# Kernel tuning notes

Measured on AMD Instinct MI355X. Metric: run time of the kernel, lower is better.

## Reference

```python
import jax, jax.numpy as jnp
import numpy as np

# Bernstein-basis theta coefficients for d=2 (calculate_theta2(2)),
# inv_coeff order: [x^0, x^1, x^2]
THETAS = ((3.0, -3.0, 0.75), (0.0, 3.0, -1.5), (0.0, 0.0, 0.75))
HIGH_ORDER = 2

N_NODES = 50000
N_EDGES = 800000
IN_DIM, HID_DIM, OUT_DIM = 128, 64, 2


def setup_inputs() -> dict:
    key = jax.random.key(0)
    ks = jax.random.split(key, 16)
    f32 = jnp.float32
    def w(k, shape, fan_in):
        return jax.random.normal(k, shape, dtype=f32) * (1.0 / np.sqrt(fan_in))
    return {
        "in_feat": jax.random.normal(ks[0], (N_NODES, IN_DIM), dtype=f32),
        "src": jax.random.randint(ks[1], (N_EDGES,), 0, N_NODES, dtype=jnp.int32),
        "dst": jax.random.randint(ks[2], (N_EDGES,), 0, N_NODES, dtype=jnp.int32),
        "W1": w(ks[3], (IN_DIM, HID_DIM), IN_DIM), "b1": jnp.zeros((HID_DIM,), f32),
        "W2": w(ks[4], (HID_DIM, HID_DIM), HID_DIM), "b2": jnp.zeros((HID_DIM,), f32),
        "W3": w(ks[5], (HID_DIM * 5, HID_DIM), HID_DIM * 5), "b3": jnp.zeros((HID_DIM,), f32),
        "W4": w(ks[6], (HID_DIM, OUT_DIM), HID_DIM), "b4": jnp.zeros((OUT_DIM,), f32),
        "Wg1": w(ks[7], (IN_DIM, HID_DIM), IN_DIM), "bg1": jnp.zeros((HID_DIM,), f32),
        "Wg2": w(ks[8], (HID_DIM, IN_DIM), HID_DIM), "bg2": jnp.zeros((IN_DIM,), f32),
    }


def _spmm(x, src, dst, n):
    # y[v] = sum_{(u,v) in E} x[u]   (DGL update_all(copy_u, sum))
    return jax.ops.segment_sum(x[src], dst, num_segments=n)


def reference(in_feat, src, dst, W1, b1, W2, b2, W3, b3, W4, b4, Wg1, bg1, Wg2, bg2):
    n = in_feat.shape[0]
    ones_e = jnp.ones(src.shape[0], dtype=in_feat.dtype)
    deg_in = jnp.clip(jax.ops.segment_sum(ones_e, dst, num_segments=n), 1.0)
    deg_out = jnp.clip(jax.ops.segment_sum(ones_e, src, num_segments=n), 1.0)
    din = (deg_in ** -0.5)[:, None]   # [N,1]
    dout = (deg_out ** -0.5)[:, None]

    def lap(f):
        # f - D^{-1/2} A D^{-1/2} f  (in-degree norm, as in unnLaplacian)
        return f - _spmm(f * din, src, dst, n) * din

    # MLP front-end
    h = jax.nn.relu(in_feat @ W1 + b1)
    h = jax.nn.relu(h @ W2 + b2)

    branches = []
    # BandConv branches (lin=False): theta-weighted Laplacian polynomial
    for theta in THETAS:
        f = h
        acc = theta[0] * h
        for k in range(1, len(theta)):
            f = lap(f)
            acc = acc + theta[k] * f
        branches.append(acc)
    # HighConv branches: repeated Laplacian, num_layer = 1..HIGH_ORDER
    f = h
    for j in range(HIGH_ORDER):
        f = lap(f)
        branches.append(f)

    h_final = jnp.concatenate(branches, axis=-1)  # [N, 5*hid]
    out = jax.nn.relu(h_final @ W3 + b3) @ W4 + b4  # [N, out_dim]

    # GCN branch on self-loop-free graph (same edges here): symmetric norm GraphConv
    def gconv(x, W, b):
        return _spmm(x * dout, src, dst, n) * din @ W + b
    emb = gconv(jax.nn.relu(gconv(in_feat, Wg1, bg1)), Wg2, bg2)  # [N, in_dim]

    return out, emb
```

## Files before the change

kernel.cpp:

```cpp
#include <hip/hip_runtime.h>
#include <hip/hip_bf16.h>
#include <math.h>

#define NN 50000
#define NE 800000
#define C64 64
#define CE 12500
#define RW2 6250
#define NW 25000
#define HISTB 256
#define INITB 160
#define RB 98
#define GB 782
#define ZSB 782
#define FSG 3125
#define FSB 6250

typedef _Float16 half8 __attribute__((ext_vector_type(8)));
typedef _Float16 half4v __attribute__((ext_vector_type(4)));
typedef float f32x4 __attribute__((ext_vector_type(4)));
typedef unsigned short ushort4v __attribute__((ext_vector_type(4)));

static inline int cdiv(int a, int b) { return (a + b - 1) / b; }


__device__ inline size_t pack_pos(int k, int n, int K, int M) {
    int tile = n >> 4;
    int kstep = k >> 5;
    int quad = (k >> 3) & 3;
    int j = k & 7;
    int lane = (quad << 4) | (n & 15);
    return ((size_t)(tile * (K >> 5) + kstep) * 64 + lane) * 8 + j;
}

__device__ void pack_std_dev(int bx, const float* __restrict__ W, _Float16* __restrict__ Wpk,
                             int K, int M) {
    int idx = bx * 256 + threadIdx.x;
    if (idx >= K * M) return;
    int k = idx / M, n = idx % M;
    Wpk[pack_pos(k, n, K, M)] = (_Float16)W[idx];
}

__device__ void pack_wc_dev(int bx, const float* __restrict__ W3, _Float16* __restrict__ wcpk) {
    int idx = bx * 256 + threadIdx.x;
    if (idx >= 3 * 4096) return;
    int b = idx >> 12;
    int rem = idx & 4095;
    int k = rem >> 6, n = rem & 63;
    float w0 = W3[(0 * 64 + k) * 64 + n];
    float w1 = W3[(1 * 64 + k) * 64 + n];
    float w2 = W3[(2 * 64 + k) * 64 + n];
    float w3 = W3[(3 * 64 + k) * 64 + n];
    float w4 = W3[(4 * 64 + k) * 64 + n];
    float v;
    if (b == 0)      v = 3.f * w0;
    else if (b == 1) v = -3.f * w0 + 3.f * w1 + w3;
    else             v = 0.75f * w0 - 1.5f * w1 + 0.75f * w2 + w4;
    wcpk[pack_pos(b * 64 + k, n, 192, 64)] = (_Float16)v;
}

__device__ void init_dev(int bx,
                         const float* __restrict__ W1, _Float16* __restrict__ W1pk,
                         const float* __restrict__ W2, _Float16* __restrict__ W2pk,
                         const float* __restrict__ Wg1, _Float16* __restrict__ Wg1pk,
                         const float* __restrict__ Wg2, _Float16* __restrict__ Wg2pk,
                         const float* __restrict__ W3, _Float16* __restrict__ wcpk) {
    if (bx < 32) { pack_std_dev(bx, W1, W1pk, 128, 64); return; }
    bx -= 32;
    if (bx < 16) { pack_std_dev(bx, W2, W2pk, 64, 64); return; }
    bx -= 16;
    if (bx < 32) { pack_std_dev(bx, Wg1, Wg1pk, 128, 64); return; }
    bx -= 32;
    if (bx < 32) { pack_std_dev(bx, Wg2, Wg2pk, 64, 128); return; }
    bx -= 32;
    pack_wc_dev(bx, W3, wcpk);
}


__device__ void hist_dev(int bx, const int* __restrict__ idx, unsigned* __restrict__ H,
                         unsigned* __restrict__ cnt) {
    int c = bx & 63, r = bx >> 6;
    int tid = threadIdx.x;
    for (int j = tid; j < RW2; j += 256) cnt[j] = 0;
    __syncthreads();
    int lo = r * 12500;
    const int* p = idx + (size_t)c * CE;
    for (int i = tid; i < CE; i += 256) {
        int v = p[i] - lo;
        if ((unsigned)v < 12500u)
            atomicAdd(&cnt[v >> 1], 1u << ((v & 1) * 16));
    }
    __syncthreads();
    unsigned* outp = H + (size_t)c * NW + r * RW2;
    for (int j = tid; j < RW2; j += 256) outp[j] = cnt[j];
}

__device__ void reduce_dev(int bx, const unsigned* __restrict__ H, int* __restrict__ dgo,
                           float* __restrict__ o_rsq, float* __restrict__ o_inv,
                           float* __restrict__ o_sq) {
    int w = bx * 256 + threadIdx.x;
    if (w >= NW) return;
    unsigned slo = 0, shi = 0;
#pragma unroll 8
    for (int c = 0; c < C64; c++) {
        unsigned h = H[(size_t)c * NW + w];
        slo += h & 0xffffu; shi += h >> 16;
    }
    if (dgo) {
        dgo[2 * w]     = slo > 64u ? 64 : (int)slo;
        dgo[2 * w + 1] = shi > 64u ? 64 : (int)shi;
    }
    float f0 = (float)(slo < 1u ? 1u : slo);
    float f1 = (float)(shi < 1u ? 1u : shi);
    o_rsq[2 * w] = rsqrtf(f0); o_rsq[2 * w + 1] = rsqrtf(f1);
    if (o_inv) { o_inv[2 * w] = 1.f / f0; o_inv[2 * w + 1] = 1.f / f1; }
    if (o_sq)  { o_sq[2 * w] = sqrtf(f0); o_sq[2 * w + 1] = sqrtf(f1); }
}

__device__ void prefix_dev(int bx, const unsigned* __restrict__ HD, unsigned* __restrict__ baseD) {
    int w = bx * 256 + threadIdx.x;
    if (w >= NW) return;
    unsigned slo = 0, shi = 0;
    for (int c = 0; c < C64; c++) {
        unsigned b0 = slo > 64u ? 64u : slo;
        unsigned b1 = shi > 64u ? 64u : shi;
        baseD[(size_t)c * NW + w] = b0 | (b1 << 16);
        unsigned h = HD[(size_t)c * NW + w];
        slo += h & 0xffffu; shi += h >> 16;
    }
}

__device__ void scatter_dev(int bx, const int* __restrict__ src, const int* __restrict__ dst,
                            const unsigned* __restrict__ baseD,
                            unsigned short* __restrict__ colsPad,
                            unsigned* __restrict__ cnt) {
    int c = bx & 63, r = bx >> 6;
    int tid = threadIdx.x;
    const unsigned* bslice = baseD + (size_t)c * NW + r * RW2;
    for (int j = tid; j < RW2; j += 256) cnt[j] = bslice[j];
    __syncthreads();
    int lo = r * 12500;
    const int* pd = dst + (size_t)c * CE;
    const int* ps = src + (size_t)c * CE;
    for (int i = tid; i < CE; i += 256) {
        int v = pd[i];
        int lv = v - lo;
        if ((unsigned)lv < 12500u) {
            int sh = (lv & 1) * 16;
            unsigned old = atomicAdd(&cnt[lv >> 1], 1u << sh);
            unsigned pos = (old >> sh) & 0xffffu;
            if (pos < 64u) colsPad[(size_t)v * 64 + pos] = (unsigned short)ps[i];
        }
    }
}

__device__ void zscale_dev(int bx, half8* __restrict__ zh8, const float* __restrict__ dout, int N) {
    int idx = bx * 256 + threadIdx.x;
    if (idx >= N * 4) return;
    int row = idx >> 2;
    float m = dout[row];
    half8 a = zh8[idx * 2], b = zh8[idx * 2 + 1];
#pragma unroll
    for (int j = 0; j < 8; j++) {
        a[j] = (_Float16)((float)a[j] * m);
        b[j] = (_Float16)((float)b[j] * m);
    }
    zh8[idx * 2] = a; zh8[idx * 2 + 1] = b;
}


struct HSegs { const _Float16* p[3]; int ld[3]; };

template <int M, int K, bool OUTW, bool RSCA>
__device__ void mg_dev(int bx, HSegs A, const half8* __restrict__ Wpk,
                       const float* __restrict__ bias, int relu,
                       float* __restrict__ C,
                       _Float16* __restrict__ Ch0, const float* __restrict__ ms0,
                       const float* __restrict__ rsc,
                       const float* __restrict__ W4, const float* __restrict__ b4,
                       float* __restrict__ outp, int N) {
    constexpr int NT = M / 16;
    constexpr int NKS = K / 32;
    int tid = threadIdx.x;
    int wave = tid >> 6, lane = tid & 63;
    int quad = lane >> 4, m = lane & 15;
    int row0 = bx * 64 + wave * 16;
    int rowA = row0 + m; if (rowA >= N) rowA = N - 1;
    _Float16 hs = (_Float16)1.f;
    if (RSCA) hs = (_Float16)rsc[rowA];
    f32x4 acc[NT];
#pragma unroll
    for (int t = 0; t < NT; t++) acc[t] = (f32x4){0.f, 0.f, 0.f, 0.f};
#pragma unroll
    for (int ks = 0; ks < NKS; ks++) {
        const _Float16* ap = A.p[ks >> 1] + (size_t)rowA * A.ld[ks >> 1] + (ks & 1) * 32 + quad * 8;
        half8 af = *(const half8*)ap;
        if (RSCA) {
#pragma unroll
            for (int j = 0; j < 8; j++) af[j] *= hs;
        }
#pragma unroll
        for (int t = 0; t < NT; t++) {
            half8 bf = Wpk[(t * NKS + ks) * 64 + lane];
            acc[t] = __builtin_amdgcn_mfma_f32_16x16x32_f16(af, bf, acc[t], 0, 0, 0);
        }
    }
    float outv[NT][4];
#pragma unroll
    for (int t = 0; t < NT; t++) {
        float bv = bias ? bias[t * 16 + m] : 0.f;
#pragma unroll
        for (int r = 0; r < 4; r++) {
            float v = acc[t][r] + bv;
            if (relu) v = fmaxf(v, 0.f);
            outv[t][r] = v;
        }
    }
    if (OUTW) {
        float w40[NT], w41[NT];
#pragma unroll
        for (int t = 0; t < NT; t++) {
            w40[t] = W4[(t * 16 + m) * 2];
            w41[t] = W4[(t * 16 + m) * 2 + 1];
        }
#pragma unroll
        for (int r = 0; r < 4; r++) {
            float p0 = 0.f, p1 = 0.f;
#pragma unroll
            for (int t = 0; t < NT; t++) {
                p0 += outv[t][r] * w40[t];
                p1 += outv[t][r] * w41[t];
            }
#pragma unroll
            for (int off = 1; off < 16; off <<= 1) {
                p0 += __shfl_xor(p0, off);
                p1 += __shfl_xor(p1, off);
            }
            int row = row0 + quad * 4 + r;
            if (m == 0 && row < N) {
                outp[(size_t)row * 2 + 0] = p0 + b4[0];
                outp[(size_t)row * 2 + 1] = p1 + b4[1];
            }
        }
    }
    if (C || Ch0) {
#pragma unroll
        for (int r = 0; r < 4; r++) {
            int row = row0 + quad * 4 + r;
            if (row >= N) continue;
            float m0 = (Ch0 && ms0) ? ms0[row] : 1.f;
#pragma unroll
            for (int t = 0; t < NT; t++) {
                size_t off = (size_t)row * M + t * 16 + m;
                if (C)   C[off] = outv[t][r];
                if (Ch0) Ch0[off] = (_Float16)(outv[t][r] * m0);
            }
        }
    }
}

__device__ void a15_dev(int bx, const float* __restrict__ in_feat,
                        const half8* __restrict__ W1pk, const half8* __restrict__ Wg1pk,
                        const float* __restrict__ b1,
                        _Float16* __restrict__ h1h, _Float16* __restrict__ zh, int N) {
    int tid = threadIdx.x;
    int wave = tid >> 6, lane = tid & 63;
    int quad = lane >> 4, m = lane & 15;
    int row0 = bx * 64 + wave * 16;
    int rowA = row0 + m; if (rowA >= N) rowA = N - 1;
    f32x4 acc0[4], acc1[4];
#pragma unroll
    for (int t = 0; t < 4; t++) {
        acc0[t] = (f32x4){0.f, 0.f, 0.f, 0.f};
        acc1[t] = (f32x4){0.f, 0.f, 0.f, 0.f};
    }
#pragma unroll
    for (int ks = 0; ks < 4; ks++) {
        const float* ap = in_feat + (size_t)rowA * 128 + ks * 32 + quad * 8;
        float4 u = *(const float4*)ap;
        float4 v = *(const float4*)(ap + 4);
        half8 af;
        af[0] = (_Float16)u.x; af[1] = (_Float16)u.y; af[2] = (_Float16)u.z; af[3] = (_Float16)u.w;
        af[4] = (_Float16)v.x; af[5] = (_Float16)v.y; af[6] = (_Float16)v.z; af[7] = (_Float16)v.w;
#pragma unroll
        for (int t = 0; t < 4; t++) {
            acc0[t] = __builtin_amdgcn_mfma_f32_16x16x32_f16(af, W1pk[(t * 4 + ks) * 64 + lane], acc0[t], 0, 0, 0);
            acc1[t] = __builtin_amdgcn_mfma_f32_16x16x32_f16(af, Wg1pk[(t * 4 + ks) * 64 + lane], acc1[t], 0, 0, 0);
        }
    }
#pragma unroll
    for (int r = 0; r < 4; r++) {
        int row = row0 + quad * 4 + r;
        if (row >= N) continue;
#pragma unroll
        for (int t = 0; t < 4; t++) {
            float v0 = fmaxf(acc0[t][r] + b1[t * 16 + m], 0.f);
            h1h[(size_t)row * 64 + t * 16 + m] = (_Float16)v0;
            zh[(size_t)row * 64 + t * 16 + m] = (_Float16)acc1[t][r];
        }
    }
}


__launch_bounds__(256)
__global__ void k_L1(const float* __restrict__ W1, _Float16* __restrict__ W1pk,
                     const float* __restrict__ W2, _Float16* __restrict__ W2pk,
                     const float* __restrict__ Wg1, _Float16* __restrict__ Wg1pk,
                     const float* __restrict__ Wg2, _Float16* __restrict__ Wg2pk,
                     const float* __restrict__ W3, _Float16* __restrict__ wcpk,
                     const int* __restrict__ src, const int* __restrict__ dst,
                     unsigned* __restrict__ HD, unsigned* __restrict__ HS) {
    __shared__ unsigned cnt[RW2];
    int bx = blockIdx.x;
    if (bx < INITB) { init_dev(bx, W1, W1pk, W2, W2pk, Wg1, Wg1pk, Wg2, Wg2pk, W3, wcpk); return; }
    bx -= INITB;
    if (bx < HISTB) { hist_dev(bx, dst, HD, cnt); return; }
    bx -= HISTB;
    hist_dev(bx, src, HS, cnt);
}

__launch_bounds__(256)
__global__ void k_L2(const unsigned* __restrict__ HD, const unsigned* __restrict__ HS,
                     int* __restrict__ degin, float* __restrict__ din,
                     float* __restrict__ din2, float* __restrict__ dsq,
                     float* __restrict__ dout, unsigned* __restrict__ baseD,
                     const float* __restrict__ in_feat,
                     const half8* __restrict__ W1pk, const half8* __restrict__ Wg1pk,
                     const float* __restrict__ b1,
                     _Float16* __restrict__ h1h, _Float16* __restrict__ zh, int N) {
    int bx = blockIdx.x;
    if (bx < RB) { reduce_dev(bx, HD, degin, din, din2, dsq); return; }
    bx -= RB;
    if (bx < RB) { reduce_dev(bx, HS, nullptr, dout, nullptr, nullptr); return; }
    bx -= RB;
    if (bx < RB) { prefix_dev(bx, HD, baseD); return; }
    bx -= RB;
    a15_dev(bx, in_feat, W1pk, Wg1pk, b1, h1h, zh, N);
}

__launch_bounds__(256)
__global__ void k_L3(const int* __restrict__ src, const int* __restrict__ dst,
                     const unsigned* __restrict__ baseD, unsigned short* __restrict__ colsPad,
                     const _Float16* __restrict__ h1h, const half8* __restrict__ W2pk,
                     const float* __restrict__ b2, _Float16* __restrict__ u0h,
                     const float* __restrict__ din,
                     half8* __restrict__ zh8, const float* __restrict__ dout, int N) {
    __shared__ unsigned cnt[RW2];
    int bx = blockIdx.x;
    if (bx < HISTB) { scatter_dev(bx, src, dst, baseD, colsPad, cnt); return; }
    bx -= HISTB;
    if (bx < GB) {
        HSegs A;
        A.p[0] = h1h; A.ld[0] = 64;
        A.p[1] = nullptr; A.ld[1] = 0;
        A.p[2] = nullptr; A.ld[2] = 0;
        mg_dev<64, 64, false, false>(bx, A, W2pk, b2, 1, nullptr, u0h, din,
                                     nullptr, nullptr, nullptr, nullptr, N);
        return;
    }
    bx -= GB;
    zscale_dev(bx, zh8, dout, N);
}


struct SpmmP {
    const half4v* xh; const half4v* fsub_h; const float* rowscale; const float* bias;
    half4v* yh0; const float* ms0; int relu;
};

__launch_bounds__(256)
__global__ void k_FS(SpmmP P0, SpmmP P1, const unsigned short* __restrict__ colsPad,
                     const int* __restrict__ deg, int N) {
    int bx = blockIdx.x;
    bool first = bx < FSG;
    SpmmP P = first ? P0 : P1;
    int g = first ? bx : bx - FSG;
    int tid = threadIdx.x;
    int wave = tid >> 6, lane = tid & 63;
    int quad = lane >> 4, c = lane & 15;
    int row = g * 16 + wave * 4 + quad;
    if (row >= N) return;
    int dg = deg[row];
    const unsigned short* cp = colsPad + (size_t)row * 64;
    float ax = 0.f, ay = 0.f, az = 0.f, aw = 0.f;
    int e = 0;
    for (; e + 7 < dg; e += 8) {
        ushort4v sa = *(const ushort4v*)(cp + e);
        ushort4v sb = *(const ushort4v*)(cp + e + 4);
        half4v v0 = P.xh[(size_t)sa.x * 16 + c];
        half4v v1 = P.xh[(size_t)sa.y * 16 + c];
        half4v v2 = P.xh[(size_t)sa.z * 16 + c];
        half4v v3 = P.xh[(size_t)sa.w * 16 + c];
        half4v v4 = P.xh[(size_t)sb.x * 16 + c];
        half4v v5 = P.xh[(size_t)sb.y * 16 + c];
        half4v v6 = P.xh[(size_t)sb.z * 16 + c];
        half4v v7 = P.xh[(size_t)sb.w * 16 + c];
        ax += (float)v0.x + (float)v1.x + (float)v2.x + (float)v3.x
            + (float)v4.x + (float)v5.x + (float)v6.x + (float)v7.x;
        ay += (float)v0.y + (float)v1.y + (float)v2.y + (float)v3.y
            + (float)v4.y + (float)v5.y + (float)v6.y + (float)v7.y;
        az += (float)v0.z + (float)v1.z + (float)v2.z + (float)v3.z
            + (float)v4.z + (float)v5.z + (float)v6.z + (float)v7.z;
        aw += (float)v0.w + (float)v1.w + (float)v2.w + (float)v3.w
            + (float)v4.w + (float)v5.w + (float)v6.w + (float)v7.w;
    }
    for (; e + 3 < dg; e += 4) {
        ushort4v ss = *(const ushort4v*)(cp + e);
        half4v v0 = P.xh[(size_t)ss.x * 16 + c];
        half4v v1 = P.xh[(size_t)ss.y * 16 + c];
        half4v v2 = P.xh[(size_t)ss.z * 16 + c];
        half4v v3 = P.xh[(size_t)ss.w * 16 + c];
        ax += (float)v0.x + (float)v1.x + (float)v2.x + (float)v3.x;
        ay += (float)v0.y + (float)v1.y + (float)v2.y + (float)v3.y;
        az += (float)v0.z + (float)v1.z + (float)v2.z + (float)v3.z;
        aw += (float)v0.w + (float)v1.w + (float)v2.w + (float)v3.w;
    }
    for (; e < dg; e++) {
        int s = cp[e];
        half4v v = P.xh[(size_t)s * 16 + c];
        ax += (float)v.x; ay += (float)v.y; az += (float)v.z; aw += (float)v.w;
    }
    size_t oidx = (size_t)row * 16 + c;
    if (P.fsub_h) {
        float d = P.rowscale[row];
        half4v f = P.fsub_h[oidx];
        ax = (float)f.x - ax * d; ay = (float)f.y - ay * d;
        az = (float)f.z - az * d; aw = (float)f.w - aw * d;
    } else {
        if (P.rowscale) { float d = P.rowscale[row]; ax *= d; ay *= d; az *= d; aw *= d; }
        if (P.bias) {
            float4 bb = ((const float4*)P.bias)[c];
            ax += bb.x; ay += bb.y; az += bb.z; aw += bb.w;
        }
        if (P.relu) {
            ax = fmaxf(ax, 0.f); ay = fmaxf(ay, 0.f);
            az = fmaxf(az, 0.f); aw = fmaxf(aw, 0.f);
        }
    }
    float mm = P.ms0 ? P.ms0[row] : 1.f;
    half4v h;
    h.x = (_Float16)(ax * mm); h.y = (_Float16)(ay * mm);
    h.z = (_Float16)(az * mm); h.w = (_Float16)(aw * mm);
    P.yh0[oidx] = h;
}

__launch_bounds__(256)
__global__ void k_F3(const _Float16* __restrict__ u0h, const _Float16* __restrict__ u1h,
                     const _Float16* __restrict__ u2h, const half8* __restrict__ wcpk,
                     const float* __restrict__ b3, const float* __restrict__ dsq,
                     const float* __restrict__ W4, const float* __restrict__ b4,
                     float* __restrict__ outp,
                     const _Float16* __restrict__ sgh, const half8* __restrict__ Wg2pk,
                     const float* __restrict__ bg2, float* __restrict__ emb, int N) {
    int bx = blockIdx.x;
    if (bx < GB) {
        HSegs A;
        A.p[0] = u0h; A.ld[0] = 64;
        A.p[1] = u1h; A.ld[1] = 64;
        A.p[2] = u2h; A.ld[2] = 64;
        mg_dev<64, 192, true, true>(bx, A, wcpk, b3, 1, nullptr, nullptr, nullptr,
                                    dsq, W4, b4, outp, N);
        return;
    }
    bx -= GB;
    HSegs A;
    A.p[0] = sgh; A.ld[0] = 64;
    A.p[1] = nullptr; A.ld[1] = 0;
    A.p[2] = nullptr; A.ld[2] = 0;
    mg_dev<128, 64, false, false>(bx, A, Wg2pk, bg2, 0, emb, nullptr, nullptr,
                                  nullptr, nullptr, nullptr, nullptr, N);
}

extern "C" void kernel_launch(void* const* d_in, const int* in_sizes, int n_in,
                              void* d_out, int out_size, void* d_ws, size_t ws_size,
                              hipStream_t stream) {
    const int N = NN;
    const float* in_feat = (const float*)d_in[0];
    const int* src = (const int*)d_in[1];
    const int* dst = (const int*)d_in[2];
    const float* W1 = (const float*)d_in[3];
    const float* b1 = (const float*)d_in[4];
    const float* W2 = (const float*)d_in[5];
    const float* b2 = (const float*)d_in[6];
    const float* W3 = (const float*)d_in[7];
    const float* b3 = (const float*)d_in[8];
    const float* W4 = (const float*)d_in[9];
    const float* b4 = (const float*)d_in[10];
    const float* Wg1 = (const float*)d_in[11];
    const float* bg1 = (const float*)d_in[12];
    const float* Wg2 = (const float*)d_in[13];
    const float* bg2 = (const float*)d_in[14];

    float* out = (float*)d_out;
    float* emb = out + (size_t)N * 2;

    float* fw = (float*)d_ws;
    float* din  = fw;
    float* din2 = din + N;
    float* dsq  = din2 + N;
    float* dout = dsq + N;
    int* degin  = (int*)(dout + N);
    unsigned short* colsPad = (unsigned short*)(degin + N);
    unsigned* HD   = (unsigned*)(colsPad + (size_t)64 * N);
    unsigned* HS   = HD + (size_t)C64 * NW;
    unsigned* baseD = HS + (size_t)C64 * NW;
    _Float16* hp = (_Float16*)(baseD + (size_t)C64 * NW);
    _Float16* h1h   = hp;
    _Float16* u0h   = h1h + (size_t)64 * N;
    _Float16* u1h   = u0h + (size_t)64 * N;
    _Float16* u2h   = u1h + (size_t)64 * N;
    _Float16* zh    = u2h + (size_t)64 * N;
    _Float16* g1h   = zh + (size_t)64 * N;
    _Float16* sgh   = g1h + (size_t)64 * N;
    _Float16* W1pk  = sgh + (size_t)64 * N;
    _Float16* W2pk  = W1pk + 8192;
    _Float16* Wg1pk = W2pk + 4096;
    _Float16* Wg2pk = Wg1pk + 8192;
    _Float16* wcpk  = Wg2pk + 8192;

    k_L1<<<INITB + 2 * HISTB, 256, 0, stream>>>(W1, W1pk, W2, W2pk, Wg1, Wg1pk,
        Wg2, Wg2pk, W3, wcpk, src, dst, HD, HS);

    k_L2<<<3 * RB + GB, 256, 0, stream>>>(HD, HS, degin, din, din2, dsq, dout, baseD,
        in_feat, (const half8*)W1pk, (const half8*)Wg1pk, b1, h1h, zh, N);

    k_L3<<<HISTB + GB + ZSB, 256, 0, stream>>>(src, dst, baseD, colsPad,
        h1h, (const half8*)W2pk, b2, u0h, din, (half8*)zh, dout, N);

    SpmmP p0, p1;
    p0 = {(const half4v*)u0h, (const half4v*)u0h, din2, nullptr, (half4v*)u1h, nullptr, 0};
    p1 = {(const half4v*)zh, nullptr, din, bg1, (half4v*)g1h, dout, 1};
    k_FS<<<FSB, 256, 0, stream>>>(p0, p1, colsPad, degin, N);

    p0 = {(const half4v*)u1h, (const half4v*)u1h, din2, nullptr, (half4v*)u2h, nullptr, 0};
    p1 = {(const half4v*)g1h, nullptr, nullptr, nullptr, (half4v*)sgh, din, 0};
    k_FS<<<FSB, 256, 0, stream>>>(p0, p1, colsPad, degin, N);

    k_F3<<<2 * GB, 256, 0, stream>>>(u0h, u1h, u2h, (const half8*)wcpk, b3, dsq,
        W4, b4, out, sgh, (const half8*)Wg2pk, bg2, emb, N);
}
```

Before: 259.4 us.

## Build padded CSR with global atomics instead of chunked LDS histograms

Replaces the multi-pass adjacency build (per-chunk LDS histograms for in- and out-degree, a 64-chunk reduction, a prefix pass and a chunked LDS scatter) with one pass over the edges. Each thread does global atomicAdd on per-node in- and out-degree counters and writes the source index into the padded column slot returned by the dst atomic. The large intermediate histogram and base arrays are removed. The kernel that used to run the scatter now runs only the GEMM and zscale work, and a memset is added to zero the counters. In exchange, neighbour order within each row becomes nondeterministic, and the build depends on global-atomic throughput and on contention for high-degree nodes.

```diff
diff --git a/kernel.cpp b/kernel.cpp
--- a/kernel.cpp
+++ b/kernel.cpp
@@ -4,13 +4,9 @@
 
 #define NN 50000
 #define NE 800000
-#define C64 64
-#define CE 12500
-#define RW2 6250
-#define NW 25000
-#define HISTB 256
+#define BLD 3125
+#define NORMB 196
 #define INITB 160
-#define RB 98
 #define GB 782
 #define ZSB 782
 #define FSG 3125
@@ -77,81 +73,32 @@
 }
 
 
-__device__ void hist_dev(int bx, const int* __restrict__ idx, unsigned* __restrict__ H,
-                         unsigned* __restrict__ cnt) {
-    int c = bx & 63, r = bx >> 6;
-    int tid = threadIdx.x;
-    for (int j = tid; j < RW2; j += 256) cnt[j] = 0;
-    __syncthreads();
-    int lo = r * 12500;
-    const int* p = idx + (size_t)c * CE;
-    for (int i = tid; i < CE; i += 256) {
-        int v = p[i] - lo;
-        if ((unsigned)v < 12500u)
-            atomicAdd(&cnt[v >> 1], 1u << ((v & 1) * 16));
-    }
-    __syncthreads();
-    unsigned* outp = H + (size_t)c * NW + r * RW2;
-    for (int j = tid; j < RW2; j += 256) outp[j] = cnt[j];
-}
-
-__device__ void reduce_dev(int bx, const unsigned* __restrict__ H, int* __restrict__ dgo,
-                           float* __restrict__ o_rsq, float* __restrict__ o_inv,
-                           float* __restrict__ o_sq) {
-    int w = bx * 256 + threadIdx.x;
-    if (w >= NW) return;
-    unsigned slo = 0, shi = 0;
-#pragma unroll 8
-    for (int c = 0; c < C64; c++) {
-        unsigned h = H[(size_t)c * NW + w];
-        slo += h & 0xffffu; shi += h >> 16;
-    }
-    if (dgo) {
-        dgo[2 * w]     = slo > 64u ? 64 : (int)slo;
-        dgo[2 * w + 1] = shi > 64u ? 64 : (int)shi;
-    }
-    float f0 = (float)(slo < 1u ? 1u : slo);
-    float f1 = (float)(shi < 1u ? 1u : shi);
-    o_rsq[2 * w] = rsqrtf(f0); o_rsq[2 * w + 1] = rsqrtf(f1);
-    if (o_inv) { o_inv[2 * w] = 1.f / f0; o_inv[2 * w + 1] = 1.f / f1; }
-    if (o_sq)  { o_sq[2 * w] = sqrtf(f0); o_sq[2 * w + 1] = sqrtf(f1); }
-}
-
-__device__ void prefix_dev(int bx, const unsigned* __restrict__ HD, unsigned* __restrict__ baseD) {
-    int w = bx * 256 + threadIdx.x;
-    if (w >= NW) return;
-    unsigned slo = 0, shi = 0;
-    for (int c = 0; c < C64; c++) {
-        unsigned b0 = slo > 64u ? 64u : slo;
-        unsigned b1 = shi > 64u ? 64u : shi;
-        baseD[(size_t)c * NW + w] = b0 | (b1 << 16);
-        unsigned h = HD[(size_t)c * NW + w];
-        slo += h & 0xffffu; shi += h >> 16;
-    }
-}
-
-__device__ void scatter_dev(int bx, const int* __restrict__ src, const int* __restrict__ dst,
-                            const unsigned* __restrict__ baseD,
-                            unsigned short* __restrict__ colsPad,
-                            unsigned* __restrict__ cnt) {
-    int c = bx & 63, r = bx >> 6;
-    int tid = threadIdx.x;
-    const unsigned* bslice = baseD + (size_t)c * NW + r * RW2;
-    for (int j = tid; j < RW2; j += 256) cnt[j] = bslice[j];
-    __syncthreads();
-    int lo = r * 12500;
-    const int* pd = dst + (size_t)c * CE;
-    const int* ps = src + (size_t)c * CE;
-    for (int i = tid; i < CE; i += 256) {
-        int v = pd[i];
-        int lv = v - lo;
-        if ((unsigned)lv < 12500u) {
-            int sh = (lv & 1) * 16;
-            unsigned old = atomicAdd(&cnt[lv >> 1], 1u << sh);
-            unsigned pos = (old >> sh) & 0xffffu;
-            if (pos < 64u) colsPad[(size_t)v * 64 + pos] = (unsigned short)ps[i];
-        }
-    }
+__device__ void build_dev(int bx, const int* __restrict__ src, const int* __restrict__ dst,
+                          int* __restrict__ cntD, int* __restrict__ cntS,
+                          unsigned short* __restrict__ colsPad) {
+    int i = bx * 256 + threadIdx.x;
+    int s = src[i];
+    int v = dst[i];
+    atomicAdd(&cntS[s], 1);
+    int pos = atomicAdd(&cntD[v], 1);
+    if (pos < 64) colsPad[(size_t)v * 64 + pos] = (unsigned short)s;
+}
+
+__device__ void norm_dev(int bx, const int* __restrict__ cntD, const int* __restrict__ cntS,
+                         int* __restrict__ degin, float* __restrict__ din,
+                         float* __restrict__ din2, float* __restrict__ dsq,
+                         float* __restrict__ dout) {
+    int i = bx * 256 + threadIdx.x;
+    if (i >= NN) return;
+    int d = cntD[i];
+    degin[i] = d > 64 ? 64 : d;
+    float f = (float)(d < 1 ? 1 : d);
+    din[i] = rsqrtf(f);
+    din2[i] = 1.f / f;
+    dsq[i] = sqrtf(f);
+    int o = cntS[i];
+    float g = (float)(o < 1 ? 1 : o);
+    dout[i] = rsqrtf(g);
 }
 
 __device__ void zscale_dev(int bx, half8* __restrict__ zh8, const float* __restrict__ dout, int N) {
@@ -303,52 +250,41 @@
 
 
 __launch_bounds__(256)
-__global__ void k_L1(const float* __restrict__ W1, _Float16* __restrict__ W1pk,
-                     const float* __restrict__ W2, _Float16* __restrict__ W2pk,
-                     const float* __restrict__ Wg1, _Float16* __restrict__ Wg1pk,
-                     const float* __restrict__ Wg2, _Float16* __restrict__ Wg2pk,
-                     const float* __restrict__ W3, _Float16* __restrict__ wcpk,
-                     const int* __restrict__ src, const int* __restrict__ dst,
-                     unsigned* __restrict__ HD, unsigned* __restrict__ HS) {
-    __shared__ unsigned cnt[RW2];
+__global__ void k_B(const float* __restrict__ W1, _Float16* __restrict__ W1pk,
+                    const float* __restrict__ W2, _Float16* __restrict__ W2pk,
+                    const float* __restrict__ Wg1, _Float16* __restrict__ Wg1pk,
+                    const float* __restrict__ Wg2, _Float16* __restrict__ Wg2pk,
+                    const float* __restrict__ W3, _Float16* __restrict__ wcpk,
+                    const int* __restrict__ src, const int* __restrict__ dst,
+                    int* __restrict__ cntD, int* __restrict__ cntS,
+                    unsigned short* __restrict__ colsPad) {
     int bx = blockIdx.x;
     if (bx < INITB) { init_dev(bx, W1, W1pk, W2, W2pk, Wg1, Wg1pk, Wg2, Wg2pk, W3, wcpk); return; }
     bx -= INITB;
-    if (bx < HISTB) { hist_dev(bx, dst, HD, cnt); return; }
-    bx -= HISTB;
-    hist_dev(bx, src, HS, cnt);
+    build_dev(bx, src, dst, cntD, cntS, colsPad);
 }
 
 __launch_bounds__(256)
-__global__ void k_L2(const unsigned* __restrict__ HD, const unsigned* __restrict__ HS,
+__global__ void k_L2(const int* __restrict__ cntD, const int* __restrict__ cntS,
                      int* __restrict__ degin, float* __restrict__ din,
                      float* __restrict__ din2, float* __restrict__ dsq,
-                     float* __restrict__ dout, unsigned* __restrict__ baseD,
+                     float* __restrict__ dout,
                      const float* __restrict__ in_feat,
                      const half8* __restrict__ W1pk, const half8* __restrict__ Wg1pk,
                      const float* __restrict__ b1,
                      _Float16* __restrict__ h1h, _Float16* __restrict__ zh, int N) {
     int bx = blockIdx.x;
-    if (bx < RB) { reduce_dev(bx, HD, degin, din, din2, dsq); return; }
-    bx -= RB;
-    if (bx < RB) { reduce_dev(bx, HS, nullptr, dout, nullptr, nullptr); return; }
-    bx -= RB;
-    if (bx < RB) { prefix_dev(bx, HD, baseD); return; }
-    bx -= RB;
+    if (bx < NORMB) { norm_dev(bx, cntD, cntS, degin, din, din2, dsq, dout); return; }
+    bx -= NORMB;
     a15_dev(bx, in_feat, W1pk, Wg1pk, b1, h1h, zh, N);
 }
 
 __launch_bounds__(256)
-__global__ void k_L3(const int* __restrict__ src, const int* __restrict__ dst,
-                     const unsigned* __restrict__ baseD, unsigned short* __restrict__ colsPad,
-                     const _Float16* __restrict__ h1h, const half8* __restrict__ W2pk,
+__global__ void k_L3(const _Float16* __restrict__ h1h, const half8* __restrict__ W2pk,
                      const float* __restrict__ b2, _Float16* __restrict__ u0h,
                      const float* __restrict__ din,
                      half8* __restrict__ zh8, const float* __restrict__ dout, int N) {
-    __shared__ unsigned cnt[RW2];
     int bx = blockIdx.x;
-    if (bx < HISTB) { scatter_dev(bx, src, dst, baseD, colsPad, cnt); return; }
-    bx -= HISTB;
     if (bx < GB) {
         HSegs A;
         A.p[0] = h1h; A.ld[0] = 64;
@@ -500,11 +436,10 @@
     float* dsq  = din2 + N;
     float* dout = dsq + N;
     int* degin  = (int*)(dout + N);
-    unsigned short* colsPad = (unsigned short*)(degin + N);
-    unsigned* HD   = (unsigned*)(colsPad + (size_t)64 * N);
-    unsigned* HS   = HD + (size_t)C64 * NW;
-    unsigned* baseD = HS + (size_t)C64 * NW;
-    _Float16* hp = (_Float16*)(baseD + (size_t)C64 * NW);
+    int* cntD   = degin + N;
+    int* cntS   = cntD + N;
+    unsigned short* colsPad = (unsigned short*)(cntS + N);
+    _Float16* hp = (_Float16*)(colsPad + (size_t)64 * N);
     _Float16* h1h   = hp;
     _Float16* u0h   = h1h + (size_t)64 * N;
     _Float16* u1h   = u0h + (size_t)64 * N;
@@ -518,14 +453,16 @@
     _Float16* Wg2pk = Wg1pk + 8192;
     _Float16* wcpk  = Wg2pk + 8192;
 
-    k_L1<<<INITB + 2 * HISTB, 256, 0, stream>>>(W1, W1pk, W2, W2pk, Wg1, Wg1pk,
-        Wg2, Wg2pk, W3, wcpk, src, dst, HD, HS);
-
-    k_L2<<<3 * RB + GB, 256, 0, stream>>>(HD, HS, degin, din, din2, dsq, dout, baseD,
+    hipMemsetAsync(cntD, 0, (size_t)2 * N * sizeof(int), stream);
+
+    k_B<<<INITB + BLD, 256, 0, stream>>>(W1, W1pk, W2, W2pk, Wg1, Wg1pk,
+        Wg2, Wg2pk, W3, wcpk, src, dst, cntD, cntS, colsPad);
+
+    k_L2<<<NORMB + GB, 256, 0, stream>>>(cntD, cntS, degin, din, din2, dsq, dout,
         in_feat, (const half8*)W1pk, (const half8*)Wg1pk, b1, h1h, zh, N);
 
-    k_L3<<<HISTB + GB + ZSB, 256, 0, stream>>>(src, dst, baseD, colsPad,
-        h1h, (const half8*)W2pk, b2, u0h, din, (half8*)zh, dout, N);
+    k_L3<<<GB + ZSB, 256, 0, stream>>>(h1h, (const half8*)W2pk, b2, u0h, din,
+        (half8*)zh, dout, N);
 
     SpmmP p0, p1;
     p0 = {(const half4v*)u0h, (const half4v*)u0h, din2, nullptr, (half4v*)u1h, nullptr, 0};
```

After: 278.8 us. +7.5%, slower.

## Interleave Laplacian and GCN features into paired 128-wide rows for fused SpMM gathers

Applied to the files above, without the earlier changes.

The Laplacian-chain features and the GCN features are now stored side by side in 128-wide fp16 rows. Each SpMM pass gathers both with a single 16-byte load per lane per edge, replacing two separate half-grid passes. This halves the number of gathered rows and index reads per SpMM, since the colsPad indices are now walked once for both streams. In exchange, all producers and consumers must use the new strides, and the wider per-lane accumulators raise register pressure.

```diff
diff --git a/kernel.cpp b/kernel.cpp
--- a/kernel.cpp
+++ b/kernel.cpp
@@ -14,10 +14,8 @@
 #define GB 782
 #define ZSB 782
 #define FSG 3125
-#define FSB 6250
 
 typedef _Float16 half8 __attribute__((ext_vector_type(8)));
-typedef _Float16 half4v __attribute__((ext_vector_type(4)));
 typedef float f32x4 __attribute__((ext_vector_type(4)));
 typedef unsigned short ushort4v __attribute__((ext_vector_type(4)));
 
@@ -154,18 +152,19 @@
     }
 }
 
-__device__ void zscale_dev(int bx, half8* __restrict__ zh8, const float* __restrict__ dout, int N) {
+__device__ void zscale_dev(int bx, half8* __restrict__ pair, const float* __restrict__ dout, int N) {
     int idx = bx * 256 + threadIdx.x;
     if (idx >= N * 4) return;
-    int row = idx >> 2;
+    int row = idx >> 2, q = idx & 3;
     float m = dout[row];
-    half8 a = zh8[idx * 2], b = zh8[idx * 2 + 1];
+    half8* z = pair + (size_t)row * 16 + 8 + q * 2;
+    half8 a = z[0], b = z[1];
 #pragma unroll
     for (int j = 0; j < 8; j++) {
         a[j] = (_Float16)((float)a[j] * m);
         b[j] = (_Float16)((float)b[j] * m);
     }
-    zh8[idx * 2] = a; zh8[idx * 2 + 1] = b;
+    z[0] = a; z[1] = b;
 }
 
 
@@ -178,7 +177,7 @@
                        _Float16* __restrict__ Ch0, const float* __restrict__ ms0,
                        const float* __restrict__ rsc,
                        const float* __restrict__ W4, const float* __restrict__ b4,
-                       float* __restrict__ outp, int N) {
+                       float* __restrict__ outp, int ldC, int N) {
     constexpr int NT = M / 16;
     constexpr int NKS = K / 32;
     int tid = threadIdx.x;
@@ -251,7 +250,7 @@
             float m0 = (Ch0 && ms0) ? ms0[row] : 1.f;
 #pragma unroll
             for (int t = 0; t < NT; t++) {
-                size_t off = (size_t)row * M + t * 16 + m;
+                size_t off = (size_t)row * ldC + t * 16 + m;
                 if (C)   C[off] = outv[t][r];
                 if (Ch0) Ch0[off] = (_Float16)(outv[t][r] * m0);
             }
@@ -296,7 +295,7 @@
         for (int t = 0; t < 4; t++) {
             float v0 = fmaxf(acc0[t][r] + b1[t * 16 + m], 0.f);
             h1h[(size_t)row * 64 + t * 16 + m] = (_Float16)v0;
-            zh[(size_t)row * 64 + t * 16 + m] = (_Float16)acc1[t][r];
+            zh[(size_t)row * 128 + t * 16 + m] = (_Float16)acc1[t][r];
         }
     }
 }
@@ -342,9 +341,9 @@
 __global__ void k_L3(const int* __restrict__ src, const int* __restrict__ dst,
                      const unsigned* __restrict__ baseD, unsigned short* __restrict__ colsPad,
                      const _Float16* __restrict__ h1h, const half8* __restrict__ W2pk,
-                     const float* __restrict__ b2, _Float16* __restrict__ u0h,
+                     const float* __restrict__ b2, _Float16* __restrict__ pair0h,
                      const float* __restrict__ din,
-                     half8* __restrict__ zh8, const float* __restrict__ dout, int N) {
+                     half8* __restrict__ pair0v, const float* __restrict__ dout, int N) {
     __shared__ unsigned cnt[RW2];
     int bx = blockIdx.x;
     if (bx < HISTB) { scatter_dev(bx, src, dst, baseD, colsPad, cnt); return; }
@@ -354,98 +353,104 @@
         A.p[0] = h1h; A.ld[0] = 64;
         A.p[1] = nullptr; A.ld[1] = 0;
         A.p[2] = nullptr; A.ld[2] = 0;
-        mg_dev<64, 64, false, false>(bx, A, W2pk, b2, 1, nullptr, u0h, din,
-                                     nullptr, nullptr, nullptr, nullptr, N);
+        mg_dev<64, 64, false, false>(bx, A, W2pk, b2, 1, nullptr, pair0h, din,
+                                     nullptr, nullptr, nullptr, nullptr, 128, N);
         return;
     }
     bx -= GB;
-    zscale_dev(bx, zh8, dout, N);
-}
-
-
-struct SpmmP {
-    const half4v* xh; const half4v* fsub_h; const float* rowscale; const float* bias;
-    half4v* yh0; const float* ms0; int relu;
+    zscale_dev(bx, pair0v, dout, N);
+}
+
+
+struct FSP {
+    const half8* xp;
+    half8* uOut; int uld;
+    half8* zOut; int zld;
+    const float* din2;
+    const float* zrs1;
+    const float* bgz;
+    const float* zrs2;
+    int zrelu;
 };
 
 __launch_bounds__(256)
-__global__ void k_FS(SpmmP P0, SpmmP P1, const unsigned short* __restrict__ colsPad,
+__global__ void k_FS(FSP P, const unsigned short* __restrict__ colsPad,
                      const int* __restrict__ deg, int N) {
-    int bx = blockIdx.x;
-    bool first = bx < FSG;
-    SpmmP P = first ? P0 : P1;
-    int g = first ? bx : bx - FSG;
+    int g = blockIdx.x;
     int tid = threadIdx.x;
     int wave = tid >> 6, lane = tid & 63;
-    int quad = lane >> 4, c = lane & 15;
-    int row = g * 16 + wave * 4 + quad;
+    int grp = lane >> 4, c = lane & 15;
+    int row = g * 16 + wave * 4 + grp;
     if (row >= N) return;
     int dg = deg[row];
     const unsigned short* cp = colsPad + (size_t)row * 64;
-    float ax = 0.f, ay = 0.f, az = 0.f, aw = 0.f;
+    float acc[8];
+#pragma unroll
+    for (int j = 0; j < 8; j++) acc[j] = 0.f;
     int e = 0;
     for (; e + 7 < dg; e += 8) {
         ushort4v sa = *(const ushort4v*)(cp + e);
         ushort4v sb = *(const ushort4v*)(cp + e + 4);
-        half4v v0 = P.xh[(size_t)sa.x * 16 + c];
-        half4v v1 = P.xh[(size_t)sa.y * 16 + c];
-        half4v v2 = P.xh[(size_t)sa.z * 16 + c];
-        half4v v3 = P.xh[(size_t)sa.w * 16 + c];
-        half4v v4 = P.xh[(size_t)sb.x * 16 + c];
-        half4v v5 = P.xh[(size_t)sb.y * 16 + c];
-        half4v v6 = P.xh[(size_t)sb.z * 16 + c];
-        half4v v7 = P.xh[(size_t)sb.w * 16 + c];
-        ax += (float)v0.x + (float)v1.x + (float)v2.x + (float)v3.x
-            + (float)v4.x + (float)v5.x + (float)v6.x + (float)v7.x;
-        ay += (float)v0.y + (float)v1.y + (float)v2.y + (float)v3.y
-            + (float)v4.y + (float)v5.y + (float)v6.y + (float)v7.y;
-        az += (float)v0.z + (float)v1.z + (float)v2.z + (float)v3.z
-            + (float)v4.z + (float)v5.z + (float)v6.z + (float)v7.z;
-        aw += (float)v0.w + (float)v1.w + (float)v2.w + (float)v3.w
-            + (float)v4.w + (float)v5.w + (float)v6.w + (float)v7.w;
+        half8 v0 = P.xp[(size_t)sa.x * 16 + c];
+        half8 v1 = P.xp[(size_t)sa.y * 16 + c];
+        half8 v2 = P.xp[(size_t)sa.z * 16 + c];
+        half8 v3 = P.xp[(size_t)sa.w * 16 + c];
+        half8 v4 = P.xp[(size_t)sb.x * 16 + c];
+        half8 v5 = P.xp[(size_t)sb.y * 16 + c];
+        half8 v6 = P.xp[(size_t)sb.z * 16 + c];
+        half8 v7 = P.xp[(size_t)sb.w * 16 + c];
+#pragma unroll
+        for (int j = 0; j < 8; j++) {
+            acc[j] += (float)v0[j] + (float)v1[j] + (float)v2[j] + (float)v3[j]
+                    + (float)v4[j] + (float)v5[j] + (float)v6[j] + (float)v7[j];
+        }
     }
     for (; e + 3 < dg; e += 4) {
         ushort4v ss = *(const ushort4v*)(cp + e);
-        half4v v0 = P.xh[(size_t)ss.x * 16 + c];
-        half4v v1 = P.xh[(size_t)ss.y * 16 + c];
-        half4v v2 = P.xh[(size_t)ss.z * 16 + c];
-        half4v v3 = P.xh[(size_t)ss.w * 16 + c];
-        ax += (float)v0.x + (float)v1.x + (float)v2.x + (float)v3.x;
-        ay += (float)v0.y + (float)v1.y + (float)v2.y + (float)v3.y;
-        az += (float)v0.z + (float)v1.z + (float)v2.z + (float)v3.z;
-        aw += (float)v0.w + (float)v1.w + (float)v2.w + (float)v3.w;
+        half8 v0 = P.xp[(size_t)ss.x * 16 + c];
+        half8 v1 = P.xp[(size_t)ss.y * 16 + c];
+        half8 v2 = P.xp[(size_t)ss.z * 16 + c];
+        half8 v3 = P.xp[(size_t)ss.w * 16 + c];
+#pragma unroll
+        for (int j = 0; j < 8; j++)
+            acc[j] += (float)v0[j] + (float)v1[j] + (float)v2[j] + (float)v3[j];
     }
     for (; e < dg; e++) {
         int s = cp[e];
-        half4v v = P.xh[(size_t)s * 16 + c];
-        ax += (float)v.x; ay += (float)v.y; az += (float)v.z; aw += (float)v.w;
-    }
-    size_t oidx = (size_t)row * 16 + c;
-    if (P.fsub_h) {
-        float d = P.rowscale[row];
-        half4v f = P.fsub_h[oidx];
-        ax = (float)f.x - ax * d; ay = (float)f.y - ay * d;
-        az = (float)f.z - az * d; aw = (float)f.w - aw * d;
+        half8 v = P.xp[(size_t)s * 16 + c];
+#pragma unroll
+        for (int j = 0; j < 8; j++) acc[j] += (float)v[j];
+    }
+    half8 h;
+    if (c < 8) {
+        float d = P.din2[row];
+        half8 f = P.xp[(size_t)row * 16 + c];
+#pragma unroll
+        for (int j = 0; j < 8; j++)
+            h[j] = (_Float16)((float)f[j] - acc[j] * d);
+        P.uOut[(size_t)row * P.uld + c] = h;
     } else {
-        if (P.rowscale) { float d = P.rowscale[row]; ax *= d; ay *= d; az *= d; aw *= d; }
-        if (P.bias) {
-            float4 bb = ((const float4*)P.bias)[c];
-            ax += bb.x; ay += bb.y; az += bb.z; aw += bb.w;
-        }
-        if (P.relu) {
-            ax = fmaxf(ax, 0.f); ay = fmaxf(ay, 0.f);
-            az = fmaxf(az, 0.f); aw = fmaxf(aw, 0.f);
-        }
-    }
-    float mm = P.ms0 ? P.ms0[row] : 1.f;
-    half4v h;
-    h.x = (_Float16)(ax * mm); h.y = (_Float16)(ay * mm);
-    h.z = (_Float16)(az * mm); h.w = (_Float16)(aw * mm);
-    P.yh0[oidx] = h;
+        float s1 = P.zrs1[row];
+#pragma unroll
+        for (int j = 0; j < 8; j++) acc[j] *= s1;
+        if (P.bgz) {
+            const float* bb = P.bgz + (c - 8) * 8;
+#pragma unroll
+            for (int j = 0; j < 8; j++) acc[j] += bb[j];
+        }
+        if (P.zrelu) {
+#pragma unroll
+            for (int j = 0; j < 8; j++) acc[j] = fmaxf(acc[j], 0.f);
+        }
+        float s2 = P.zrs2 ? P.zrs2[row] : 1.f;
+#pragma unroll
+        for (int j = 0; j < 8; j++) h[j] = (_Float16)(acc[j] * s2);
+        P.zOut[(size_t)row * P.zld + (c - 8)] = h;
+    }
 }
 
 __launch_bounds__(256)
-__global__ void k_F3(const _Float16* __restrict__ u0h, const _Float16* __restrict__ u1h,
+__global__ void k_F3(const _Float16* __restrict__ pair0, const _Float16* __restrict__ pair1,
                      const _Float16* __restrict__ u2h, const half8* __restrict__ wcpk,
                      const float* __restrict__ b3, const float* __restrict__ dsq,
                      const float* __restrict__ W4, const float* __restrict__ b4,
@@ -455,11 +460,11 @@
     int bx = blockIdx.x;
     if (bx < GB) {
         HSegs A;
-        A.p[0] = u0h; A.ld[0] = 64;
-        A.p[1] = u1h; A.ld[1] = 64;
-        A.p[2] = u2h; A.ld[2] = 64;
+        A.p[0] = pair0; A.ld[0] = 128;
+        A.p[1] = pair1; A.ld[1] = 128;
+        A.p[2] = u2h;   A.ld[2] = 64;
         mg_dev<64, 192, true, true>(bx, A, wcpk, b3, 1, nullptr, nullptr, nullptr,
-                                    dsq, W4, b4, outp, N);
+                                    dsq, W4, b4, outp, 64, N);
         return;
     }
     bx -= GB;
@@ -468,7 +473,7 @@
     A.p[1] = nullptr; A.ld[1] = 0;
     A.p[2] = nullptr; A.ld[2] = 0;
     mg_dev<128, 64, false, false>(bx, A, Wg2pk, bg2, 0, emb, nullptr, nullptr,
-                                  nullptr, nullptr, nullptr, nullptr, N);
+                                  nullptr, nullptr, nullptr, nullptr, 128, N);
 }
 
 extern "C" void kernel_launch(void* const* d_in, const int* in_sizes, int n_in,
@@ -506,12 +511,10 @@
     unsigned* baseD = HS + (size_t)C64 * NW;
     _Float16* hp = (_Float16*)(baseD + (size_t)C64 * NW);
     _Float16* h1h   = hp;
-    _Float16* u0h   = h1h + (size_t)64 * N;
-    _Float16* u1h   = u0h + (size_t)64 * N;
-    _Float16* u2h   = u1h + (size_t)64 * N;
-    _Float16* zh    = u2h + (size_t)64 * N;
-    _Float16* g1h   = zh + (size_t)64 * N;
-    _Float16* sgh   = g1h + (size_t)64 * N;
+    _Float16* pair0 = h1h + (size_t)64 * N;
+    _Float16* pair1 = pair0 + (size_t)128 * N;
+    _Float16* u2h   = pair1 + (size_t)128 * N;
+    _Float16* sgh   = u2h + (size_t)64 * N;
     _Float16* W1pk  = sgh + (size_t)64 * N;
     _Float16* W2pk  = W1pk + 8192;
     _Float16* Wg1pk = W2pk + 4096;
@@ -522,20 +525,20 @@
         Wg2, Wg2pk, W3, wcpk, src, dst, HD, HS);
 
     k_L2<<<3 * RB + GB, 256, 0, stream>>>(HD, HS, degin, din, din2, dsq, dout, baseD,
-        in_feat, (const half8*)W1pk, (const half8*)Wg1pk, b1, h1h, zh, N);
+        in_feat, (const half8*)W1pk, (const half8*)Wg1pk, b1, h1h, pair0 + 64, N);
 
     k_L3<<<HISTB + GB + ZSB, 256, 0, stream>>>(src, dst, baseD, colsPad,
-        h1h, (const half8*)W2pk, b2, u0h, din, (half8*)zh, dout, N);
-
-    SpmmP p0, p1;
-    p0 = {(const half4v*)u0h, (const half4v*)u0h, din2, nullptr, (half4v*)u1h, nullptr, 0};
-    p1 = {(const half4v*)zh, nullptr, din, bg1, (half4v*)g1h, dout, 1};
-    k_FS<<<FSB, 256, 0, stream>>>(p0, p1, colsPad, degin, N);
-
-    p0 = {(const half4v*)u1h, (const half4v*)u1h, din2, nullptr, (half4v*)u2h, nullptr, 0};
-    p1 = {(const half4v*)g1h, nullptr, nullptr, nullptr, (half4v*)sgh, din, 0};
-    k_FS<<<FSB, 256, 0, stream>>>(p0, p1, colsPad, degin, N);
-
-    k_F3<<<2 * GB, 256, 0, stream>>>(u0h, u1h, u2h, (const half8*)wcpk, b3, dsq,
+        h1h, (const half8*)W2pk, b2, pair0, din, (half8*)pair0, dout, N);
+
+    FSP p;
+    p = {(const half8*)pair0, (half8*)pair1, 16, (half8*)pair1 + 8, 16,
+         din2, din, bg1, dout, 1};
+    k_FS<<<FSG, 256, 0, stream>>>(p, colsPad, degin, N);
+
+    p = {(const half8*)pair1, (half8*)u2h, 8, (half8*)sgh, 8,
+         din2, din, nullptr, nullptr, 0};
+    k_FS<<<FSG, 256, 0, stream>>>(p, colsPad, degin, N);
+
+    k_F3<<<2 * GB, 256, 0, stream>>>(pair0, pair1, u2h, (const half8*)wcpk, b3, dsq,
         W4, b4, out, sgh, (const half8*)Wg2pk, bg2, emb, N);
 }
```

Result: no change. 261.3 us (+0.8%).
